# Optimization experiments

Hardware: AMD Instinct MI355X
Metric: run time of the kernel (lower is better)

The kernel has to match this reference:

```python
import jax, jax.numpy as jnp
import numpy as np

NUM_ROUNDS = 4
NUM_REVERSE_ROUNDS = 4
N_NODES = 1_000_000
N_EDGES = 32_000_000


def _scatter_mean(x, src, dst, num_nodes):
    # x: [N, F]; gather messages from src nodes, mean-reduce at dst nodes.
    msgs = x[src]                                             # [E, F]
    agg = jax.ops.segment_sum(msgs, dst, num_segments=num_nodes)  # [N, F]
    cnt = jax.ops.segment_sum(jnp.ones((src.shape[0],), x.dtype), dst,
                              num_segments=num_nodes)         # [N]
    return agg / jnp.maximum(cnt, 1.0)[:, None]


def setup_inputs() -> dict:
    key = jax.random.key(0)
    k1, k2, k3 = jax.random.split(key, 3)
    topic_one_hot = jax.random.uniform(k1, (N_NODES,), dtype=jnp.float32)
    edge_index = jax.random.randint(k2, (2, N_EDGES), 0, N_NODES, dtype=jnp.int32)
    reverse_edge_index = jax.random.randint(k3, (2, N_EDGES), 0, N_NODES, dtype=jnp.int32)
    return {
        "topic_one_hot": topic_one_hot,
        "edge_index": edge_index,
        "reverse_edge_index": reverse_edge_index,
    }


def reference(topic_one_hot, edge_index, reverse_edge_index):
    n = topic_one_hot.shape[0]
    results = []
    # forward-direction rounds
    h = topic_one_hot[:, None]  # [N, 1]
    src, dst = edge_index[0], edge_index[1]
    for _ in range(NUM_ROUNDS):
        h = _scatter_mean(h, src, dst, n)
        results.append(h)
    # reverse-direction rounds
    h_rev = topic_one_hot[:, None]
    rsrc, rdst = reverse_edge_index[0], reverse_edge_index[1]
    for _ in range(NUM_REVERSE_ROUNDS):
        h_rev = _scatter_mean(h_rev, rsrc, rdst, n)
        results.append(h_rev)
    # original returns a python list of [N,1] tensors; stack for a single array
    return jnp.stack(results, axis=0)  # [num_rounds+num_reverse_rounds, N, 1]
```

## Files before the change

### kernel.cpp

```cpp
#include <hip/hip_runtime.h>


typedef unsigned uint32x4 __attribute__((ext_vector_type(4)));

#define TPB_E 1024
#define NPART 512
#define TPB_P 512
#define BATCH 8192
#define CAP 32
#define NBMAX 512
#define BSH 11
#define BSZ 2048
#define BMASK 2047u


__global__ __launch_bounds__(TPB_P)
void p1_count(const int* __restrict__ dst, unsigned* __restrict__ blkcnt,
              int E, int chunk, int NB) {
    __shared__ unsigned h[NBMAX];
    for (int i = threadIdx.x; i < NB; i += TPB_P) h[i] = 0u;
    __syncthreads();
    int beg = blockIdx.x * chunk;
    int end = min(beg + chunk, E);
    int len = end - beg; if (len < 0) len = 0;
    const uint32x4* d4 = (const uint32x4*)(dst + beg);
    int n4 = len >> 2;
    for (int i = threadIdx.x; i < n4; i += TPB_P) {
        uint32x4 d = __builtin_nontemporal_load(&d4[i]);
        atomicAdd(&h[d.x >> BSH], 1u);
        atomicAdd(&h[d.y >> BSH], 1u);
        atomicAdd(&h[d.z >> BSH], 1u);
        atomicAdd(&h[d.w >> BSH], 1u);
    }
    __syncthreads();
    unsigned* o = blkcnt + (size_t)blockIdx.x * NB;
    for (int i = threadIdx.x; i < NB; i += TPB_P) o[i] = h[i];
}

__global__ __launch_bounds__(TPB_P)
void s1_totals(const unsigned* __restrict__ blkcnt, unsigned* __restrict__ totals,
               int NB, int nblk) {
    __shared__ unsigned red[TPB_P];
    int b = blockIdx.x;
    unsigned s = 0;
    for (int k = threadIdx.x; k < nblk; k += TPB_P) s += blkcnt[(size_t)k * NB + b];
    red[threadIdx.x] = s;
    __syncthreads();
    for (int off = TPB_P / 2; off > 0; off >>= 1) {
        if (threadIdx.x < off) red[threadIdx.x] += red[threadIdx.x + off];
        __syncthreads();
    }
    if (threadIdx.x == 0) totals[b] = red[0];
}

__global__ __launch_bounds__(TPB_P)
void s2_scan(const unsigned* __restrict__ totals, unsigned* __restrict__ base, int NB) {
    __shared__ unsigned t[TPB_P];
    int tid = threadIdx.x;
    unsigned v = (tid < NB) ? totals[tid] : 0u;
    t[tid] = v;
    __syncthreads();
    for (int off = 1; off < TPB_P; off <<= 1) {
        unsigned w = (tid >= off) ? t[tid - off] : 0u;
        __syncthreads();
        t[tid] += w;
        __syncthreads();
    }
    if (tid < NB) base[tid] = t[tid] - v;
    if (tid == NB - 1) base[NB] = t[tid];
}

__global__ __launch_bounds__(TPB_P)
void s3_start(const unsigned* __restrict__ blkcnt, const unsigned* __restrict__ base,
              unsigned* __restrict__ start, int NB, int nblk) {
    __shared__ unsigned t[TPB_P];
    int b = blockIdx.x;
    int tid = threadIdx.x;
    unsigned v = (tid < nblk) ? blkcnt[(size_t)tid * NB + b] : 0u;
    t[tid] = v;
    __syncthreads();
    for (int off = 1; off < TPB_P; off <<= 1) {
        unsigned w = (tid >= off) ? t[tid - off] : 0u;
        __syncthreads();
        t[tid] += w;
        __syncthreads();
    }
    if (tid < nblk) start[(size_t)tid * NB + b] = base[b] + t[tid] - v;
}

__global__ __launch_bounds__(TPB_P)
void p2_scatter(const int* __restrict__ src, const int* __restrict__ dst,
                const unsigned* __restrict__ start, unsigned* __restrict__ packed,
                int E, int chunk, int NB) {
    __shared__ unsigned stg[NBMAX * CAP];
    __shared__ unsigned h[NBMAX];
    __shared__ unsigned gcur[NBMAX];
    int tid = threadIdx.x;
    int bid = blockIdx.x;
    for (int i = tid; i < NB; i += TPB_P) gcur[i] = start[(size_t)bid * NB + i];
    int beg = bid * chunk;
    int end = min(beg + chunk, E);
    int wid = tid >> 6, lane = tid & 63;
    for (int bb = beg; bb < end; bb += BATCH) {
        int bend = min(bb + BATCH, end);
        int n4 = (bend - bb) >> 2;
        for (int i = tid; i < NB; i += TPB_P) h[i] = 0u;
        __syncthreads();
        const uint32x4* s4 = (const uint32x4*)(src + bb);
        const uint32x4* d4 = (const uint32x4*)(dst + bb);
        for (int i = tid; i < n4; i += TPB_P) {
            uint32x4 s = __builtin_nontemporal_load(&s4[i]);
            uint32x4 d = __builtin_nontemporal_load(&d4[i]);
            unsigned sv[4] = {s.x, s.y, s.z, s.w};
            unsigned dv[4] = {d.x, d.y, d.z, d.w};
            #pragma unroll
            for (int k = 0; k < 4; ++k) {
                unsigned b = dv[k] >> BSH;
                unsigned val = (sv[k] << BSH) | (dv[k] & BMASK);
                unsigned pos = atomicAdd(&h[b], 1u);
                if (pos < CAP) stg[(b << 5) + ((pos + b) & 31u)] = val;
                else packed[gcur[b] + pos] = val;
            }
        }
        __syncthreads();
        for (int b = wid; b < NB; b += TPB_P / 64) {
            unsigned cnt = h[b];
            unsigned n = cnt < CAP ? cnt : CAP;
            unsigned g0 = gcur[b];
            for (unsigned i = lane; i < n; i += 64)
                packed[g0 + i] = stg[(b << 5) + ((i + b) & 31u)];
            if (lane == 0) gcur[b] = g0 + cnt;
        }
        __syncthreads();
    }
}

template <bool FIRST>
__global__ __launch_bounds__(TPB_E)
void e_pass(const float* __restrict__ x, const unsigned* __restrict__ packed,
            const unsigned* __restrict__ boff, float* __restrict__ cnt,
            float* __restrict__ outslice, int N) {
    __shared__ float acc[BSZ];
    __shared__ unsigned c[FIRST ? BSZ : 1];
    int tid = threadIdx.x;
    for (int i = tid; i < BSZ; i += TPB_E) {
        acc[i] = 0.0f;
        if (FIRST) c[i] = 0u;
    }
    __syncthreads();
    int b = blockIdx.x;
    int beg = (int)boff[b], end = (int)boff[b + 1];
    int a0 = min((beg + 3) & ~3, end);
    for (int e = beg + tid; e < a0; e += TPB_E) {
        unsigned p = packed[e];
        atomicAdd(&acc[p & BMASK], x[p >> BSH]);
        if (FIRST) atomicAdd(&c[p & BMASK], 1u);
    }
    int i0 = a0 >> 2, i1 = i0 + ((end - a0) >> 2);
    const uint32x4* p4 = (const uint32x4*)packed;
    for (int i = i0 + tid; i < i1; i += TPB_E) {
        uint32x4 p = p4[i];
        float x0 = x[p.x >> BSH];
        float x1 = x[p.y >> BSH];
        float x2 = x[p.z >> BSH];
        float x3 = x[p.w >> BSH];
        atomicAdd(&acc[p.x & BMASK], x0);
        atomicAdd(&acc[p.y & BMASK], x1);
        atomicAdd(&acc[p.z & BMASK], x2);
        atomicAdd(&acc[p.w & BMASK], x3);
        if (FIRST) {
            atomicAdd(&c[p.x & BMASK], 1u);
            atomicAdd(&c[p.y & BMASK], 1u);
            atomicAdd(&c[p.z & BMASK], 1u);
            atomicAdd(&c[p.w & BMASK], 1u);
        }
    }
    for (int e = a0 + ((end - a0) & ~3) + tid; e < end; e += TPB_E) {
        unsigned p = packed[e];
        atomicAdd(&acc[p & BMASK], x[p >> BSH]);
        if (FIRST) atomicAdd(&c[p & BMASK], 1u);
    }
    __syncthreads();
    int nbase = b << BSH;
    for (int i = tid; i < BSZ; i += TPB_E) {
        int node = nbase + i;
        if (node < N) {
            float cn = FIRST ? (float)c[i] : cnt[node];
            if (FIRST) cnt[node] = cn;
            outslice[node] = acc[i] / fmaxf(cn, 1.0f);
        }
    }
}


#define TPB 256
#define MAX_BLOCKS 2048

__global__ void round_first(const float* __restrict__ x,
                            const int* __restrict__ src,
                            const int* __restrict__ dst,
                            float* __restrict__ agg,
                            float* __restrict__ cnt,
                            int nE4, int nE) {
    int i = blockIdx.x * blockDim.x + threadIdx.x;
    int stride = gridDim.x * blockDim.x;
    const int4* src4 = (const int4*)src;
    const int4* dst4 = (const int4*)dst;
    for (; i < nE4; i += stride) {
        int4 s = src4[i];
        int4 d = dst4[i];
        atomicAdd(&agg[d.x], x[s.x]); atomicAdd(&cnt[d.x], 1.0f);
        atomicAdd(&agg[d.y], x[s.y]); atomicAdd(&cnt[d.y], 1.0f);
        atomicAdd(&agg[d.z], x[s.z]); atomicAdd(&cnt[d.z], 1.0f);
        atomicAdd(&agg[d.w], x[s.w]); atomicAdd(&cnt[d.w], 1.0f);
    }
    if (blockIdx.x == 0) {
        for (int e = nE4 * 4 + threadIdx.x; e < nE; e += blockDim.x) {
            int s = src[e], d = dst[e];
            atomicAdd(&agg[d], x[s]);
            atomicAdd(&cnt[d], 1.0f);
        }
    }
}

__global__ void round_next(const float* __restrict__ x,
                           const int* __restrict__ src,
                           const int* __restrict__ dst,
                           float* __restrict__ agg,
                           int nE4, int nE) {
    int i = blockIdx.x * blockDim.x + threadIdx.x;
    int stride = gridDim.x * blockDim.x;
    const int4* src4 = (const int4*)src;
    const int4* dst4 = (const int4*)dst;
    for (; i < nE4; i += stride) {
        int4 s = src4[i];
        int4 d = dst4[i];
        atomicAdd(&agg[d.x], x[s.x]);
        atomicAdd(&agg[d.y], x[s.y]);
        atomicAdd(&agg[d.z], x[s.z]);
        atomicAdd(&agg[d.w], x[s.w]);
    }
    if (blockIdx.x == 0) {
        for (int e = nE4 * 4 + threadIdx.x; e < nE; e += blockDim.x) {
            int s = src[e], d = dst[e];
            atomicAdd(&agg[d], x[s]);
        }
    }
}

__global__ void normalize_k(float* __restrict__ out,
                            const float* __restrict__ cnt,
                            int n4, int n) {
    int i = blockIdx.x * blockDim.x + threadIdx.x;
    int stride = gridDim.x * blockDim.x;
    float4* o4 = (float4*)out;
    const float4* c4 = (const float4*)cnt;
    for (; i < n4; i += stride) {
        float4 o = o4[i];
        float4 c = c4[i];
        o.x /= fmaxf(c.x, 1.0f);
        o.y /= fmaxf(c.y, 1.0f);
        o.z /= fmaxf(c.z, 1.0f);
        o.w /= fmaxf(c.w, 1.0f);
        o4[i] = o;
    }
    if (blockIdx.x == 0) {
        for (int e = n4 * 4 + threadIdx.x; e < n; e += blockDim.x) {
            out[e] /= fmaxf(cnt[e], 1.0f);
        }
    }
}


extern "C" void kernel_launch(void* const* d_in, const int* in_sizes, int n_in,
                              void* d_out, int out_size, void* d_ws, size_t ws_size,
                              hipStream_t stream) {
    const float* topic = (const float*)d_in[0];
    const int* ei  = (const int*)d_in[1];
    const int* rei = (const int*)d_in[2];
    const int N = in_sizes[0];
    const int E = in_sizes[1] / 2;

    float* out = (float*)d_out;

    const int NB = (N + BSZ - 1) >> BSH;
    const int chunk = ((E + NPART * 16 - 1) / (NPART * 16)) * 16;

    size_t off = 0;
    auto alloc = [&](size_t bytes) { size_t o = off; off += (bytes + 255) & ~(size_t)255; return o; };
    size_t o_packed = alloc((size_t)E * 4);
    size_t o_cnt    = alloc((size_t)N * 4);
    size_t o_blkcnt = alloc((size_t)NPART * NB * 4);
    size_t o_start  = alloc((size_t)NPART * NB * 4);
    size_t o_totals = alloc((size_t)NBMAX * 4);
    size_t o_base   = alloc((size_t)(NBMAX + 1) * 4);
    bool fast = (off <= ws_size) && (NB >= 2) && (NB <= NBMAX) &&
                (N <= (1 << 20)) && (E % 16 == 0);

    if (fast) {
        char* ws = (char*)d_ws;
        unsigned* packed = (unsigned*)(ws + o_packed);
        float*    cnt    = (float*)   (ws + o_cnt);
        unsigned* blkcnt = (unsigned*)(ws + o_blkcnt);
        unsigned* start  = (unsigned*)(ws + o_start);
        unsigned* totals = (unsigned*)(ws + o_totals);
        unsigned* base   = (unsigned*)(ws + o_base);

        for (int dir = 0; dir < 2; ++dir) {
            const int* src = (dir == 0) ? ei : rei;
            const int* dst = src + E;
            float* oslab = out + (size_t)dir * 4 * N;

            p1_count<<<NPART, TPB_P, 0, stream>>>(dst, blkcnt, E, chunk, NB);
            s1_totals<<<NB, TPB_P, 0, stream>>>(blkcnt, totals, NB, NPART);
            s2_scan<<<1, TPB_P, 0, stream>>>(totals, base, NB);
            s3_start<<<NB, TPB_P, 0, stream>>>(blkcnt, base, start, NB, NPART);
            p2_scatter<<<NPART, TPB_P, 0, stream>>>(src, dst, start, packed, E, chunk, NB);

            e_pass<true><<<NB, TPB_E, 0, stream>>>(topic, packed, base, cnt, oslab, N);
            for (int r = 1; r < 4; ++r) {
                e_pass<false><<<NB, TPB_E, 0, stream>>>(oslab + (size_t)(r - 1) * N, packed,
                                                        base, cnt, oslab + (size_t)r * N, N);
            }
        }
        return;
    }

    const int* src = ei;
    const int* dst = ei + E;
    const int* rsrc = rei;
    const int* rdst = rei + E;

    float* cnt_f = (float*)d_ws;
    float* cnt_r = cnt_f + N;

    (void)hipMemsetAsync(d_out, 0, (size_t)out_size * sizeof(float), stream);
    (void)hipMemsetAsync(d_ws, 0, (size_t)2 * N * sizeof(float), stream);

    const int nE4 = E / 4;
    const int n4 = N / 4;
    int eb = (nE4 + TPB - 1) / TPB; if (eb > MAX_BLOCKS) eb = MAX_BLOCKS;
    int nb = (n4 + TPB - 1) / TPB;  if (nb > MAX_BLOCKS) nb = MAX_BLOCKS;

    round_first<<<eb, TPB, 0, stream>>>(topic, src, dst, out, cnt_f, nE4, E);
    normalize_k<<<nb, TPB, 0, stream>>>(out, cnt_f, n4, N);
    for (int r = 1; r < 4; ++r) {
        round_next<<<eb, TPB, 0, stream>>>(out + (size_t)(r - 1) * N, src, dst,
                                           out + (size_t)r * N, nE4, E);
        normalize_k<<<nb, TPB, 0, stream>>>(out + (size_t)r * N, cnt_f, n4, N);
    }
    round_first<<<eb, TPB, 0, stream>>>(topic, rsrc, rdst, out + (size_t)4 * N, cnt_r, nE4, E);
    normalize_k<<<nb, TPB, 0, stream>>>(out + (size_t)4 * N, cnt_r, n4, N);
    for (int r = 5; r < 8; ++r) {
        round_next<<<eb, TPB, 0, stream>>>(out + (size_t)(r - 1) * N, rsrc, rdst,
                                           out + (size_t)r * N, nE4, E);
        normalize_k<<<nb, TPB, 0, stream>>>(out + (size_t)r * N, cnt_r, n4, N);
    }
}
```

Before: 1.722 ms.

## Add two-level source/destination binning so gathers hit staged LDS tiles

Edges are bucketed into 4096-node destination blocks, then each block's edges are re-partitioned by 8192-node source blocks. The round kernel can then stage x tiles in LDS and gather from shared memory instead of random global loads. Counts move to a separate pass. This targets the scattered global gathers in each of the eight rounds, at the cost of an extra repartition pass, an extra E-sized buffer, and serial iteration over source tiles inside each block. Only 245 blocks are launched.

```diff
diff --git a/kernel.cpp b/kernel.cpp
--- a/kernel.cpp
+++ b/kernel.cpp
@@ -6,18 +6,22 @@
 #define TPB_E 1024
 #define NPART 512
 #define TPB_P 512
-#define BATCH 8192
-#define CAP 32
-#define NBMAX 512
-#define BSH 11
-#define BSZ 2048
-#define BMASK 2047u
+#define BATCHA 8192
+#define CAPA 64
+#define NDBMAX 256
+#define DSH 12
+#define DMASK 4095u
+#define SSH 13
+#define SMASK 8191u
+#define NSBMAX 128
+#define BATCHB 4096
+#define CAPB 64
 
 
 __global__ __launch_bounds__(TPB_P)
 void p1_count(const int* __restrict__ dst, unsigned* __restrict__ blkcnt,
               int E, int chunk, int NB) {
-    __shared__ unsigned h[NBMAX];
+    __shared__ unsigned h[NDBMAX];
     for (int i = threadIdx.x; i < NB; i += TPB_P) h[i] = 0u;
     __syncthreads();
     int beg = blockIdx.x * chunk;
@@ -27,10 +31,10 @@
     int n4 = len >> 2;
     for (int i = threadIdx.x; i < n4; i += TPB_P) {
         uint32x4 d = __builtin_nontemporal_load(&d4[i]);
-        atomicAdd(&h[d.x >> BSH], 1u);
-        atomicAdd(&h[d.y >> BSH], 1u);
-        atomicAdd(&h[d.z >> BSH], 1u);
-        atomicAdd(&h[d.w >> BSH], 1u);
+        atomicAdd(&h[d.x >> DSH], 1u);
+        atomicAdd(&h[d.y >> DSH], 1u);
+        atomicAdd(&h[d.z >> DSH], 1u);
+        atomicAdd(&h[d.w >> DSH], 1u);
     }
     __syncthreads();
     unsigned* o = blkcnt + (size_t)blockIdx.x * NB;
@@ -92,17 +96,17 @@
 void p2_scatter(const int* __restrict__ src, const int* __restrict__ dst,
                 const unsigned* __restrict__ start, unsigned* __restrict__ packed,
                 int E, int chunk, int NB) {
-    __shared__ unsigned stg[NBMAX * CAP];
-    __shared__ unsigned h[NBMAX];
-    __shared__ unsigned gcur[NBMAX];
+    __shared__ unsigned stg[NDBMAX * CAPA];
+    __shared__ unsigned h[NDBMAX];
+    __shared__ unsigned gcur[NDBMAX];
     int tid = threadIdx.x;
     int bid = blockIdx.x;
     for (int i = tid; i < NB; i += TPB_P) gcur[i] = start[(size_t)bid * NB + i];
     int beg = bid * chunk;
     int end = min(beg + chunk, E);
     int wid = tid >> 6, lane = tid & 63;
-    for (int bb = beg; bb < end; bb += BATCH) {
-        int bend = min(bb + BATCH, end);
+    for (int bb = beg; bb < end; bb += BATCHA) {
+        int bend = min(bb + BATCHA, end);
         int n4 = (bend - bb) >> 2;
         for (int i = tid; i < NB; i += TPB_P) h[i] = 0u;
         __syncthreads();
@@ -115,160 +119,192 @@
             unsigned dv[4] = {d.x, d.y, d.z, d.w};
             #pragma unroll
             for (int k = 0; k < 4; ++k) {
-                unsigned b = dv[k] >> BSH;
-                unsigned val = (sv[k] << BSH) | (dv[k] & BMASK);
+                unsigned b = dv[k] >> DSH;
+                unsigned val = (sv[k] << DSH) | (dv[k] & DMASK);
                 unsigned pos = atomicAdd(&h[b], 1u);
-                if (pos < CAP) stg[(b << 5) + ((pos + b) & 31u)] = val;
+                if (pos < CAPA) stg[(b << 6) + ((pos + b) & 63u)] = val;
                 else packed[gcur[b] + pos] = val;
             }
         }
         __syncthreads();
         for (int b = wid; b < NB; b += TPB_P / 64) {
             unsigned cnt = h[b];
-            unsigned n = cnt < CAP ? cnt : CAP;
+            unsigned n = cnt < CAPA ? cnt : CAPA;
             unsigned g0 = gcur[b];
             for (unsigned i = lane; i < n; i += 64)
-                packed[g0 + i] = stg[(b << 5) + ((i + b) & 31u)];
+                packed[g0 + i] = stg[(b << 6) + ((i + b) & 63u)];
             if (lane == 0) gcur[b] = g0 + cnt;
         }
         __syncthreads();
     }
 }
 
-template <bool FIRST>
+
 __global__ __launch_bounds__(TPB_E)
-void e_pass(const float* __restrict__ x, const unsigned* __restrict__ packed,
-            const unsigned* __restrict__ boff, float* __restrict__ cnt,
-            float* __restrict__ outslice, int N) {
-    __shared__ float acc[BSZ];
-    __shared__ unsigned c[FIRST ? BSZ : 1];
-    int tid = threadIdx.x;
-    for (int i = tid; i < BSZ; i += TPB_E) {
-        acc[i] = 0.0f;
-        if (FIRST) c[i] = 0u;
-    }
+void c_pass(const unsigned* __restrict__ packed1, const unsigned* __restrict__ base,
+            float* __restrict__ cnt, int N) {
+    __shared__ unsigned c[1 << DSH];
+    int db = blockIdx.x, tid = threadIdx.x;
+    for (int i = tid; i < (1 << DSH); i += TPB_E) c[i] = 0u;
+    __syncthreads();
+    int beg = (int)base[db], end = (int)base[db + 1];
+    for (int e = beg + tid; e < end; e += TPB_E)
+        atomicAdd(&c[packed1[e] & DMASK], 1u);
+    __syncthreads();
+    int nbase = db << DSH;
+    int nmax = min(N - nbase, 1 << DSH);
+    for (int i = tid; i < nmax; i += TPB_E) cnt[nbase + i] = (float)c[i];
+}
+
+
+__global__ __launch_bounds__(TPB_E)
+void b_repart(const unsigned* __restrict__ packed1, const unsigned* __restrict__ base,
+              unsigned* __restrict__ packed2, unsigned* __restrict__ celloff,
+              int NSB) {
+    __shared__ unsigned h[NSBMAX];
+    __shared__ unsigned gcur[NSBMAX];
+    __shared__ unsigned stg[NSBMAX * CAPB];
+    int db = blockIdx.x;
+    int tid = threadIdx.x;
+    int segbeg = (int)base[db], segend = (int)base[db + 1];
+    for (int i = tid; i < NSB; i += TPB_E) h[i] = 0u;
+    __syncthreads();
+    for (int e = segbeg + tid; e < segend; e += TPB_E)
+        atomicAdd(&h[packed1[e] >> (DSH + SSH)], 1u);
+    __syncthreads();
+    if (tid == 0) {
+        unsigned run = (unsigned)segbeg;
+        for (int i = 0; i < NSB; ++i) {
+            unsigned c = h[i];
+            gcur[i] = run;
+            celloff[(size_t)db * (NSB + 1) + i] = run;
+            run += c;
+        }
+        celloff[(size_t)db * (NSB + 1) + NSB] = run;
+    }
+    __syncthreads();
+    int wid = tid >> 6, lane = tid & 63;
+    for (int bb = segbeg; bb < segend; bb += BATCHB) {
+        int bend = min(bb + BATCHB, segend);
+        for (int i = tid; i < NSB; i += TPB_E) h[i] = 0u;
+        __syncthreads();
+        for (int e = bb + tid; e < bend; e += TPB_E) {
+            unsigned p = packed1[e];
+            unsigned sb = p >> (DSH + SSH);
+            unsigned v = (((p >> DSH) & SMASK) << DSH) | (p & DMASK);
+            unsigned pos = atomicAdd(&h[sb], 1u);
+            if (pos < CAPB) stg[(sb << 6) + ((pos + sb) & 63u)] = v;
+            else packed2[gcur[sb] + pos] = v;
+        }
+        __syncthreads();
+        for (int b = wid; b < NSB; b += TPB_E / 64) {
+            unsigned cnt = h[b];
+            unsigned n = cnt < CAPB ? cnt : CAPB;
+            unsigned g0 = gcur[b];
+            for (unsigned i = lane; i < n; i += 64)
+                packed2[g0 + i] = stg[(b << 6) + ((i + b) & 63u)];
+            if (lane == 0) gcur[b] = g0 + cnt;
+        }
+        __syncthreads();
+    }
+}
+
+
+__global__ __launch_bounds__(TPB_E)
+void t_pass(const float* __restrict__ x, const unsigned* __restrict__ packed2,
+            const unsigned* __restrict__ celloff, const float* __restrict__ cnt,
+            float* __restrict__ outslice, int N, int NSB) {
+    __shared__ float xt[1 << SSH];
+    __shared__ float acc[1 << DSH];
+    int tid = threadIdx.x;
+    int db = blockIdx.x;
+    for (int i = tid; i < (1 << DSH); i += TPB_E) acc[i] = 0.0f;
+    const unsigned* co = celloff + (size_t)db * (NSB + 1);
+    for (int sb = 0; sb < NSB; ++sb) {
+        __syncthreads();
+        int tbase = sb << SSH;
+        int navail = min(N - tbase, 1 << SSH);
+        int n4 = navail >> 2;
+        const float4* x4 = (const float4*)(x + tbase);
+        for (int i = tid; i < n4; i += TPB_E) ((float4*)xt)[i] = x4[i];
+        for (int i = (n4 << 2) + tid; i < navail; i += TPB_E) xt[i] = x[tbase + i];
+        for (int i = navail + tid; i < (1 << SSH); i += TPB_E) xt[i] = 0.0f;
+        __syncthreads();
+        int beg = (int)co[sb], end = (int)co[sb + 1];
+        for (int e = beg + tid; e < end; e += TPB_E) {
+            unsigned p = __builtin_nontemporal_load(&packed2[e]);
+            atomicAdd(&acc[p & DMASK], xt[p >> DSH]);
+        }
+    }
+    __syncthreads();
+    int nbase = db << DSH;
+    int nmax = min(N - nbase, 1 << DSH);
+    for (int i = tid; i < nmax; i += TPB_E)
+        outslice[nbase + i] = acc[i] / fmaxf(cnt[nbase + i], 1.0f);
+}
+
+
+__global__ __launch_bounds__(TPB_E)
+void e_pass12(const float* __restrict__ x, const unsigned* __restrict__ packed,
+              const unsigned* __restrict__ boff, const float* __restrict__ cnt,
+              float* __restrict__ outslice, int N) {
+    __shared__ float acc[1 << DSH];
+    int tid = threadIdx.x;
+    for (int i = tid; i < (1 << DSH); i += TPB_E) acc[i] = 0.0f;
     __syncthreads();
     int b = blockIdx.x;
     int beg = (int)boff[b], end = (int)boff[b + 1];
     int a0 = min((beg + 3) & ~3, end);
     for (int e = beg + tid; e < a0; e += TPB_E) {
         unsigned p = packed[e];
-        atomicAdd(&acc[p & BMASK], x[p >> BSH]);
-        if (FIRST) atomicAdd(&c[p & BMASK], 1u);
+        atomicAdd(&acc[p & DMASK], x[p >> DSH]);
     }
     int i0 = a0 >> 2, i1 = i0 + ((end - a0) >> 2);
     const uint32x4* p4 = (const uint32x4*)packed;
     for (int i = i0 + tid; i < i1; i += TPB_E) {
         uint32x4 p = p4[i];
-        float x0 = x[p.x >> BSH];
-        float x1 = x[p.y >> BSH];
-        float x2 = x[p.z >> BSH];
-        float x3 = x[p.w >> BSH];
-        atomicAdd(&acc[p.x & BMASK], x0);
-        atomicAdd(&acc[p.y & BMASK], x1);
-        atomicAdd(&acc[p.z & BMASK], x2);
-        atomicAdd(&acc[p.w & BMASK], x3);
-        if (FIRST) {
-            atomicAdd(&c[p.x & BMASK], 1u);
-            atomicAdd(&c[p.y & BMASK], 1u);
-            atomicAdd(&c[p.z & BMASK], 1u);
-            atomicAdd(&c[p.w & BMASK], 1u);
-        }
+        atomicAdd(&acc[p.x & DMASK], x[p.x >> DSH]);
+        atomicAdd(&acc[p.y & DMASK], x[p.y >> DSH]);
+        atomicAdd(&acc[p.z & DMASK], x[p.z >> DSH]);
+        atomicAdd(&acc[p.w & DMASK], x[p.w >> DSH]);
     }
     for (int e = a0 + ((end - a0) & ~3) + tid; e < end; e += TPB_E) {
         unsigned p = packed[e];
-        atomicAdd(&acc[p & BMASK], x[p >> BSH]);
-        if (FIRST) atomicAdd(&c[p & BMASK], 1u);
-    }
-    __syncthreads();
-    int nbase = b << BSH;
-    for (int i = tid; i < BSZ; i += TPB_E) {
-        int node = nbase + i;
-        if (node < N) {
-            float cn = FIRST ? (float)c[i] : cnt[node];
-            if (FIRST) cnt[node] = cn;
-            outslice[node] = acc[i] / fmaxf(cn, 1.0f);
-        }
-    }
+        atomicAdd(&acc[p & DMASK], x[p >> DSH]);
+    }
+    __syncthreads();
+    int nbase = b << DSH;
+    int nmax = min(N - nbase, 1 << DSH);
+    for (int i = tid; i < nmax; i += TPB_E)
+        outslice[nbase + i] = acc[i] / fmaxf(cnt[nbase + i], 1.0f);
 }
 
 
 #define TPB 256
 #define MAX_BLOCKS 2048
 
-__global__ void round_first(const float* __restrict__ x,
-                            const int* __restrict__ src,
-                            const int* __restrict__ dst,
-                            float* __restrict__ agg,
-                            float* __restrict__ cnt,
-                            int nE4, int nE) {
+__global__ void round_first(const float* __restrict__ x, const int* __restrict__ src,
+                            const int* __restrict__ dst, float* __restrict__ agg,
+                            float* __restrict__ cnt, int nE) {
     int i = blockIdx.x * blockDim.x + threadIdx.x;
     int stride = gridDim.x * blockDim.x;
-    const int4* src4 = (const int4*)src;
-    const int4* dst4 = (const int4*)dst;
-    for (; i < nE4; i += stride) {
-        int4 s = src4[i];
-        int4 d = dst4[i];
-        atomicAdd(&agg[d.x], x[s.x]); atomicAdd(&cnt[d.x], 1.0f);
-        atomicAdd(&agg[d.y], x[s.y]); atomicAdd(&cnt[d.y], 1.0f);
-        atomicAdd(&agg[d.z], x[s.z]); atomicAdd(&cnt[d.z], 1.0f);
-        atomicAdd(&agg[d.w], x[s.w]); atomicAdd(&cnt[d.w], 1.0f);
-    }
-    if (blockIdx.x == 0) {
-        for (int e = nE4 * 4 + threadIdx.x; e < nE; e += blockDim.x) {
-            int s = src[e], d = dst[e];
-            atomicAdd(&agg[d], x[s]);
-            atomicAdd(&cnt[d], 1.0f);
-        }
-    }
-}
-
-__global__ void round_next(const float* __restrict__ x,
-                           const int* __restrict__ src,
-                           const int* __restrict__ dst,
-                           float* __restrict__ agg,
-                           int nE4, int nE) {
+    for (; i < nE; i += stride) {
+        atomicAdd(&agg[dst[i]], x[src[i]]);
+        atomicAdd(&cnt[dst[i]], 1.0f);
+    }
+}
+
+__global__ void round_next(const float* __restrict__ x, const int* __restrict__ src,
+                           const int* __restrict__ dst, float* __restrict__ agg, int nE) {
     int i = blockIdx.x * blockDim.x + threadIdx.x;
     int stride = gridDim.x * blockDim.x;
-    const int4* src4 = (const int4*)src;
-    const int4* dst4 = (const int4*)dst;
-    for (; i < nE4; i += stride) {
-        int4 s = src4[i];
-        int4 d = dst4[i];
-        atomicAdd(&agg[d.x], x[s.x]);
-        atomicAdd(&agg[d.y], x[s.y]);
-        atomicAdd(&agg[d.z], x[s.z]);
-        atomicAdd(&agg[d.w], x[s.w]);
-    }
-    if (blockIdx.x == 0) {
-        for (int e = nE4 * 4 + threadIdx.x; e < nE; e += blockDim.x) {
-            int s = src[e], d = dst[e];
-            atomicAdd(&agg[d], x[s]);
-        }
-    }
-}
-
-__global__ void normalize_k(float* __restrict__ out,
-                            const float* __restrict__ cnt,
-                            int n4, int n) {
+    for (; i < nE; i += stride) atomicAdd(&agg[dst[i]], x[src[i]]);
+}
+
+__global__ void normalize_k(float* __restrict__ out, const float* __restrict__ cnt, int n) {
     int i = blockIdx.x * blockDim.x + threadIdx.x;
     int stride = gridDim.x * blockDim.x;
-    float4* o4 = (float4*)out;
-    const float4* c4 = (const float4*)cnt;
-    for (; i < n4; i += stride) {
-        float4 o = o4[i];
-        float4 c = c4[i];
-        o.x /= fmaxf(c.x, 1.0f);
-        o.y /= fmaxf(c.y, 1.0f);
-        o.z /= fmaxf(c.z, 1.0f);
-        o.w /= fmaxf(c.w, 1.0f);
-        o4[i] = o;
-    }
-    if (blockIdx.x == 0) {
-        for (int e = n4 * 4 + threadIdx.x; e < n; e += blockDim.x) {
-            out[e] /= fmaxf(cnt[e], 1.0f);
-        }
-    }
+    for (; i < n; i += stride) out[i] /= fmaxf(cnt[i], 1.0f);
 }
 
 
@@ -283,43 +319,60 @@
 
     float* out = (float*)d_out;
 
-    const int NB = (N + BSZ - 1) >> BSH;
+    const int NDB = (N + (int)DMASK) >> DSH;
+    const int NSB = (N + (int)SMASK) >> SSH;
     const int chunk = ((E + NPART * 16 - 1) / (NPART * 16)) * 16;
 
     size_t off = 0;
     auto alloc = [&](size_t bytes) { size_t o = off; off += (bytes + 255) & ~(size_t)255; return o; };
-    size_t o_packed = alloc((size_t)E * 4);
-    size_t o_cnt    = alloc((size_t)N * 4);
-    size_t o_blkcnt = alloc((size_t)NPART * NB * 4);
-    size_t o_start  = alloc((size_t)NPART * NB * 4);
-    size_t o_totals = alloc((size_t)NBMAX * 4);
-    size_t o_base   = alloc((size_t)(NBMAX + 1) * 4);
-    bool fast = (off <= ws_size) && (NB >= 2) && (NB <= NBMAX) &&
-                (N <= (1 << 20)) && (E % 16 == 0);
-
-    if (fast) {
+    size_t o_packed1 = alloc((size_t)E * 4);
+    size_t o_cnt     = alloc((size_t)N * 4);
+    size_t o_blkcnt  = alloc((size_t)NPART * NDB * 4);
+    size_t o_start   = alloc((size_t)NPART * NDB * 4);
+    size_t o_base    = alloc((size_t)(NDBMAX + 1) * 4);
+    size_t need_mid  = off;
+    size_t o_packed2 = alloc((size_t)E * 4);
+    size_t o_celloff = alloc((size_t)NDB * (NSB + 1) * 4);
+    size_t need_2d   = off;
+
+    bool shapes_ok = (NDB >= 2) && (NDB <= NDBMAX) && (NSB >= 1) && (NSB <= NSBMAX) &&
+                     (N <= (1 << 20)) && (E % 16 == 0) && (E > 0);
+    bool full = shapes_ok && (need_2d <= ws_size);
+    bool mid  = shapes_ok && (need_mid <= ws_size);
+
+    if (full || mid) {
         char* ws = (char*)d_ws;
-        unsigned* packed = (unsigned*)(ws + o_packed);
-        float*    cnt    = (float*)   (ws + o_cnt);
-        unsigned* blkcnt = (unsigned*)(ws + o_blkcnt);
-        unsigned* start  = (unsigned*)(ws + o_start);
-        unsigned* totals = (unsigned*)(ws + o_totals);
-        unsigned* base   = (unsigned*)(ws + o_base);
+        unsigned* packed1 = (unsigned*)(ws + o_packed1);
+        float*    cnt     = (float*)   (ws + o_cnt);
+        unsigned* blkcnt  = (unsigned*)(ws + o_blkcnt);
+        unsigned* start   = (unsigned*)(ws + o_start);
+        unsigned* base    = (unsigned*)(ws + o_base);
+        unsigned* packed2 = full ? (unsigned*)(ws + o_packed2) : nullptr;
+        unsigned* celloff = full ? (unsigned*)(ws + o_celloff) : nullptr;
 
         for (int dir = 0; dir < 2; ++dir) {
             const int* src = (dir == 0) ? ei : rei;
             const int* dst = src + E;
             float* oslab = out + (size_t)dir * 4 * N;
 
-            p1_count<<<NPART, TPB_P, 0, stream>>>(dst, blkcnt, E, chunk, NB);
-            s1_totals<<<NB, TPB_P, 0, stream>>>(blkcnt, totals, NB, NPART);
-            s2_scan<<<1, TPB_P, 0, stream>>>(totals, base, NB);
-            s3_start<<<NB, TPB_P, 0, stream>>>(blkcnt, base, start, NB, NPART);
-            p2_scatter<<<NPART, TPB_P, 0, stream>>>(src, dst, start, packed, E, chunk, NB);
-
-            e_pass<true><<<NB, TPB_E, 0, stream>>>(topic, packed, base, cnt, oslab, N);
-            for (int r = 1; r < 4; ++r) {
-                e_pass<false><<<NB, TPB_E, 0, stream>>>(oslab + (size_t)(r - 1) * N, packed,
+            p1_count<<<NPART, TPB_P, 0, stream>>>(dst, blkcnt, E, chunk, NDB);
+            s1_totals<<<NDB, TPB_P, 0, stream>>>(blkcnt, start, NDB, NPART);
+            s2_scan<<<1, TPB_P, 0, stream>>>(start, base, NDB);
+            s3_start<<<NDB, TPB_P, 0, stream>>>(blkcnt, base, start, NDB, NPART);
+            p2_scatter<<<NPART, TPB_P, 0, stream>>>(src, dst, start, packed1, E, chunk, NDB);
+
+            c_pass<<<NDB, TPB_E, 0, stream>>>(packed1, base, cnt, N);
+
+            if (full) {
+                b_repart<<<NDB, TPB_E, 0, stream>>>(packed1, base, packed2, celloff, NSB);
+                t_pass<<<NDB, TPB_E, 0, stream>>>(topic, packed2, celloff, cnt, oslab, N, NSB);
+                for (int r = 1; r < 4; ++r)
+                    t_pass<<<NDB, TPB_E, 0, stream>>>(oslab + (size_t)(r - 1) * N, packed2,
+                                                      celloff, cnt, oslab + (size_t)r * N, N, NSB);
+            } else {
+                e_pass12<<<NDB, TPB_E, 0, stream>>>(topic, packed1, base, cnt, oslab, N);
+                for (int r = 1; r < 4; ++r)
+                    e_pass12<<<NDB, TPB_E, 0, stream>>>(oslab + (size_t)(r - 1) * N, packed1,
                                                         base, cnt, oslab + (size_t)r * N, N);
             }
         }
@@ -337,23 +390,21 @@
     (void)hipMemsetAsync(d_out, 0, (size_t)out_size * sizeof(float), stream);
     (void)hipMemsetAsync(d_ws, 0, (size_t)2 * N * sizeof(float), stream);
 
-    const int nE4 = E / 4;
-    const int n4 = N / 4;
-    int eb = (nE4 + TPB - 1) / TPB; if (eb > MAX_BLOCKS) eb = MAX_BLOCKS;
-    int nb = (n4 + TPB - 1) / TPB;  if (nb > MAX_BLOCKS) nb = MAX_BLOCKS;
-
-    round_first<<<eb, TPB, 0, stream>>>(topic, src, dst, out, cnt_f, nE4, E);
-    normalize_k<<<nb, TPB, 0, stream>>>(out, cnt_f, n4, N);
+    int eb = (E + TPB - 1) / TPB; if (eb > MAX_BLOCKS) eb = MAX_BLOCKS;
+    int nb = (N + TPB - 1) / TPB; if (nb > MAX_BLOCKS) nb = MAX_BLOCKS;
+
+    round_first<<<eb, TPB, 0, stream>>>(topic, src, dst, out, cnt_f, E);
+    normalize_k<<<nb, TPB, 0, stream>>>(out, cnt_f, N);
     for (int r = 1; r < 4; ++r) {
         round_next<<<eb, TPB, 0, stream>>>(out + (size_t)(r - 1) * N, src, dst,
-                                           out + (size_t)r * N, nE4, E);
-        normalize_k<<<nb, TPB, 0, stream>>>(out + (size_t)r * N, cnt_f, n4, N);
-    }
-    round_first<<<eb, TPB, 0, stream>>>(topic, rsrc, rdst, out + (size_t)4 * N, cnt_r, nE4, E);
-    normalize_k<<<nb, TPB, 0, stream>>>(out + (size_t)4 * N, cnt_r, n4, N);
+                                           out + (size_t)r * N, E);
+        normalize_k<<<nb, TPB, 0, stream>>>(out + (size_t)r * N, cnt_f, N);
+    }
+    round_first<<<eb, TPB, 0, stream>>>(topic, rsrc, rdst, out + (size_t)4 * N, cnt_r, E);
+    normalize_k<<<nb, TPB, 0, stream>>>(out + (size_t)4 * N, cnt_r, N);
     for (int r = 5; r < 8; ++r) {
         round_next<<<eb, TPB, 0, stream>>>(out + (size_t)(r - 1) * N, rsrc, rdst,
-                                           out + (size_t)r * N, nE4, E);
-        normalize_k<<<nb, TPB, 0, stream>>>(out + (size_t)r * N, cnt_r, n4, N);
-    }
-}
+                                           out + (size_t)r * N, E);
+        normalize_k<<<nb, TPB, 0, stream>>>(out + (size_t)r * N, cnt_r, N);
+    }
+}
```

Measured after the change: 2.869 ms. 1.67x slower.
